# Performance work log

Hardware: AMD Instinct MI355X
Metric: run time of the kernel (lower is better)

The kernel has to match this reference:

```python
import jax, jax.numpy as jnp
import numpy as np

TEMPERATURE = 0.05
EPS = 1e-8  # torch.nn.CosineSimilarity eps


def setup_inputs() -> dict:
    key = jax.random.key(0)
    k1, k2 = jax.random.split(key)
    z1 = jax.random.normal(k1, (8192, 512), dtype=jnp.float32)
    z2 = jax.random.normal(k2, (8192, 512), dtype=jnp.float32)
    return {"z1": z1, "z2": z2}


def reference(z1, z2):
    # Pairwise cosine similarity via GEMM on raw dots / outer product of norms,
    # matching torch CosineSimilarity: dot / max(||a||*||b||, eps).
    dots = jnp.einsum('id,jd->ij', z1, z2)          # [N, N]
    n1 = jnp.linalg.norm(z1, axis=-1)               # [N]
    n2 = jnp.linalg.norm(z2, axis=-1)               # [N]
    denom = jnp.maximum(n1[:, None] * n2[None, :], EPS)
    sim = dots / denom / TEMPERATURE                # [N, N]
    return -jnp.mean(jax.scipy.special.logsumexp(sim, axis=-1))
```

## Files before the change

kernel.cpp:

```cpp
#include <hip/hip_runtime.h>
#include <hip/hip_bf16.h>

#define NROW 8192
#define DDIM 512
#define TEMP_INV 20.0f
#define SHIFT 20.0f

#define BM 256
#define BN 256
#define BK 64
#define KT (DDIM / BK)
#define TILE_A_ELE (BM * BK)
#define BUF_ELE (2 * TILE_A_ELE)
#define LDS_BYTES (2 * BUF_ELE * 2)

typedef __attribute__((ext_vector_type(8))) short short8;
typedef __attribute__((ext_vector_type(4))) float f32x4;

__device__ __forceinline__ void gload16(const __hip_bfloat16* g, __hip_bfloat16* l) {
  __builtin_amdgcn_global_load_lds(
      (const __attribute__((address_space(1))) void*)g,
      (__attribute__((address_space(3))) void*)l,
      16, 0, 0);
}

__global__ __launch_bounds__(256) void normalize_rows(
    const float* __restrict__ z1, const float* __restrict__ z2,
    __hip_bfloat16* __restrict__ z1n, __hip_bfloat16* __restrict__ z2n,
    float* __restrict__ rowsum) {
  int row = blockIdx.x * 4 + (threadIdx.x >> 6);
  int lane = threadIdx.x & 63;

  const float* src;
  __hip_bfloat16* dst;
  float numer;
  if (row < NROW) {
    src = z1 + (size_t)row * DDIM;
    dst = z1n + (size_t)row * DDIM;
    numer = TEMP_INV;
    if (lane == 0) rowsum[row] = 0.0f;
  } else {
    int r = row - NROW;
    src = z2 + (size_t)r * DDIM;
    dst = z2n + (size_t)r * DDIM;
    numer = 1.0f;
  }

  float4 v0 = *reinterpret_cast<const float4*>(src + lane * 8);
  float4 v1 = *reinterpret_cast<const float4*>(src + lane * 8 + 4);
  float ss = v0.x * v0.x + v0.y * v0.y + v0.z * v0.z + v0.w * v0.w +
             v1.x * v1.x + v1.y * v1.y + v1.z * v1.z + v1.w * v1.w;
#pragma unroll
  for (int off = 32; off; off >>= 1) ss += __shfl_xor(ss, off);

  float scale = numer / fmaxf(sqrtf(ss), 1e-8f);

  float vals[8] = {v0.x, v0.y, v0.z, v0.w, v1.x, v1.y, v1.z, v1.w};
  union { __hip_bfloat16 h[8]; uint4 q; } pk;
#pragma unroll
  for (int j = 0; j < 8; ++j) pk.h[j] = __float2bfloat16(vals[j] * scale);
  *reinterpret_cast<uint4*>(dst + lane * 8) = pk.q;
}

#define VMC(N) asm volatile("s_waitcnt vmcnt(" #N ")" ::: "memory")
#define SBAR()                          \
  do {                                  \
    __builtin_amdgcn_s_barrier();       \
    __builtin_amdgcn_sched_barrier(0);  \
  } while (0)

#define LDSA(BUFB, QM, MI, KK)                                                \
  (*reinterpret_cast<const short8*>(                                          \
      &lds[(size_t)(BUFB) * BUF_ELE +                                         \
           (wr * 128 + (QM) * 64 + (MI) * 16 + l15) * BK +                    \
           ((((KK) * 4 + hi) ^ x7) * 8)]))
#define LDSB(BUFB, QN, NI, KK)                                                \
  (*reinterpret_cast<const short8*>(                                          \
      &lds[(size_t)(BUFB) * BUF_ELE + TILE_A_ELE +                            \
           (wc * 64 + (QN) * 32 + (NI) * 16 + l15) * BK +                     \
           ((((KK) * 4 + hi) ^ x7) * 8)]))

#define MF4(QM, MI, QN, BF)                                                   \
  acc[(QM) * 4 + (MI)][(QN) * 2 + 0] =                                        \
      __builtin_amdgcn_mfma_f32_16x16x32_bf16(                                \
          af[(MI) * 2 + 0], (BF)[0], acc[(QM) * 4 + (MI)][(QN) * 2 + 0],      \
          0, 0, 0);                                                           \
  acc[(QM) * 4 + (MI)][(QN) * 2 + 0] =                                        \
      __builtin_amdgcn_mfma_f32_16x16x32_bf16(                                \
          af[(MI) * 2 + 1], (BF)[1], acc[(QM) * 4 + (MI)][(QN) * 2 + 0],      \
          0, 0, 0);                                                           \
  acc[(QM) * 4 + (MI)][(QN) * 2 + 1] =                                        \
      __builtin_amdgcn_mfma_f32_16x16x32_bf16(                                \
          af[(MI) * 2 + 0], (BF)[2], acc[(QM) * 4 + (MI)][(QN) * 2 + 1],      \
          0, 0, 0);                                                           \
  acc[(QM) * 4 + (MI)][(QN) * 2 + 1] =                                        \
      __builtin_amdgcn_mfma_f32_16x16x32_bf16(                                \
          af[(MI) * 2 + 1], (BF)[3], acc[(QM) * 4 + (MI)][(QN) * 2 + 1],      \
          0, 0, 0);

#define PHASE_A(BUFB, QM, ST, H)                                              \
  do {                                                                        \
    af[0] = LDSA(BUFB, QM, 0, 0); af[1] = LDSA(BUFB, QM, 0, 1);               \
    af[2] = LDSA(BUFB, QM, 1, 0); af[3] = LDSA(BUFB, QM, 1, 1);               \
    STAGE_HALF(ST, H);                                                        \
    af[4] = LDSA(BUFB, QM, 2, 0); af[5] = LDSA(BUFB, QM, 2, 1);               \
    af[6] = LDSA(BUFB, QM, 3, 0); af[7] = LDSA(BUFB, QM, 3, 1);               \
    SBAR();                                                                   \
    __builtin_amdgcn_s_setprio(1);                                            \
    MF4(QM, 0, 0, bf0) MF4(QM, 1, 0, bf0)                                     \
    MF4(QM, 2, 0, bf0) MF4(QM, 3, 0, bf0)                                     \
    __builtin_amdgcn_s_setprio(0);                                            \
    SBAR();                                                                   \
  } while (0)

#define PHASE_B(BUFB, ST, H)                                                  \
  do {                                                                        \
    bf1[0] = LDSB(BUFB, 1, 0, 0); bf1[1] = LDSB(BUFB, 1, 0, 1);               \
    bf1[2] = LDSB(BUFB, 1, 1, 0); bf1[3] = LDSB(BUFB, 1, 1, 1);               \
    STAGE_HALF(ST, H);                                                        \
    SBAR();                                                                   \
    __builtin_amdgcn_s_setprio(1);                                            \
    MF4(0, 0, 1, bf1) MF4(0, 1, 1, bf1)                                       \
    MF4(0, 2, 1, bf1) MF4(0, 3, 1, bf1)                                       \
    __builtin_amdgcn_s_setprio(0);                                            \
    SBAR();                                                                   \
  } while (0)

#define PHASE_W(ST, PBUF)                                                     \
  do {                                                                        \
    STAGE_HALF(ST, 0);                                                        \
    VMC(2);                                                                   \
    SBAR();                                                                   \
    bf0[0] = LDSB(PBUF, 0, 0, 0); bf0[1] = LDSB(PBUF, 0, 0, 1);               \
    bf0[2] = LDSB(PBUF, 0, 1, 0); bf0[3] = LDSB(PBUF, 0, 1, 1);               \
    __builtin_amdgcn_s_setprio(1);                                            \
    MF4(1, 0, 1, bf1) MF4(1, 1, 1, bf1)                                       \
    MF4(1, 2, 1, bf1) MF4(1, 3, 1, bf1)                                       \
    __builtin_amdgcn_s_setprio(0);                                            \
    SBAR();                                                                   \
  } while (0)

__global__ __launch_bounds__(512, 2) void gemm_lse(
    const __hip_bfloat16* __restrict__ An,
    const __hip_bfloat16* __restrict__ Bn,
    float* __restrict__ rowsum) {
  extern __shared__ __align__(16) __hip_bfloat16 lds[];

  const int bid = blockIdx.x;
  const int chunk = bid & 7;
  const int slot = bid >> 3;
  const int by = chunk * 4 + ((slot >> 2) & 3);
  const int bx = (slot >> 4) * 4 + (slot & 3);
  const int brow = by * BM;
  const int bcol = bx * BN;

  const int tid = threadIdx.x;
  const int w = tid >> 6;
  const int lane = tid & 63;
  const int wr = w >> 2;
  const int wc = w & 3;

  f32x4 acc[8][4];
#pragma unroll
  for (int m = 0; m < 8; ++m)
#pragma unroll
    for (int n = 0; n < 4; ++n) acc[m][n] = (f32x4)0.0f;

  const int srow8 = lane >> 3;
  const int sslot = (lane & 7) ^ srow8;

  auto STAGE_HALF = [&](int st, int h) {
    const int stm = st & (KT - 1);
    const __hip_bfloat16* gbase =
        (h < 2) ? An + (size_t)brow * DDIM : Bn + (size_t)bcol * DDIM;
    const int rowt = (h & 1) * 128 + w * 16;
    const __hip_bfloat16* g =
        gbase + (size_t)(rowt + srow8) * DDIM + stm * BK + sslot * 8;
    __hip_bfloat16* dst = lds + (size_t)(stm & 1) * BUF_ELE +
                          ((h >= 2) ? TILE_A_ELE : 0) + rowt * BK;
    gload16(g, dst);
    gload16(g + (size_t)8 * DDIM, dst + 8 * BK);
  };

  const int hi = lane >> 4;
  const int l15 = lane & 15;
  const int x7 = lane & 7;

  STAGE_HALF(0, 0); STAGE_HALF(0, 1); STAGE_HALF(0, 2); STAGE_HALF(0, 3);
  STAGE_HALF(1, 0);
  VMC(2);
  SBAR();

  short8 af[8], bf0[4], bf1[4];
  bf0[0] = LDSB(0, 0, 0, 0); bf0[1] = LDSB(0, 0, 0, 1);
  bf0[2] = LDSB(0, 0, 1, 0); bf0[3] = LDSB(0, 0, 1, 1);

  for (int i = 0; i < KT / 2; ++i) {
    const int t1 = 2 * i + 1, t2 = 2 * i + 2, t3 = 2 * i + 3;
    PHASE_A(0, 0, t1, 1);
    PHASE_B(0, t1, 2);
    PHASE_A(0, 1, t1, 3);
    PHASE_W(t2, 1);
    PHASE_A(1, 0, t2, 1);
    PHASE_B(1, t2, 2);
    PHASE_A(1, 1, t2, 3);
    PHASE_W(t3, 0);
  }

  const float L2E = 1.4426950408889634f;
  const float NEG = -SHIFT * 1.4426950408889634f;
#pragma unroll
  for (int m = 0; m < 8; ++m) {
#pragma unroll
    for (int r = 0; r < 4; ++r) {
      float s = 0.0f;
#pragma unroll
      for (int n = 0; n < 4; ++n)
        s += exp2f(fmaf(acc[m][n][r], L2E, NEG));
      s += __shfl_xor(s, 1);
      s += __shfl_xor(s, 2);
      s += __shfl_xor(s, 4);
      s += __shfl_xor(s, 8);
      if (l15 == 0)
        atomicAdd(&rowsum[brow + wr * 128 + m * 16 + hi * 4 + r], s);
    }
  }
}

__global__ __launch_bounds__(1024) void finalize_lse(
    const float* __restrict__ rowsum, float* __restrict__ out) {
  __shared__ float sm[16];
  float s = 0.0f;
  for (int i = threadIdx.x; i < NROW; i += 1024) s += logf(rowsum[i]);
#pragma unroll
  for (int off = 32; off; off >>= 1) s += __shfl_xor(s, off);
  int w = threadIdx.x >> 6;
  if ((threadIdx.x & 63) == 0) sm[w] = s;
  __syncthreads();
  if (threadIdx.x == 0) {
    float t = 0.0f;
#pragma unroll
    for (int i = 0; i < 16; ++i) t += sm[i];
    out[0] = -(t / (float)NROW + SHIFT);
  }
}

extern "C" void kernel_launch(void* const* d_in, const int* in_sizes, int n_in,
                              void* d_out, int out_size, void* d_ws,
                              size_t ws_size, hipStream_t stream) {
  const float* z1 = (const float*)d_in[0];
  const float* z2 = (const float*)d_in[1];
  float* out = (float*)d_out;

  char* ws = (char*)d_ws;
  __hip_bfloat16* z1n = (__hip_bfloat16*)ws;
  __hip_bfloat16* z2n = (__hip_bfloat16*)(ws + (size_t)NROW * DDIM * 2);
  float* rowsum = (float*)(ws + (size_t)2 * NROW * DDIM * 2);

  static bool attr_set = false;
  if (!attr_set) {
    hipFuncSetAttribute((const void*)gemm_lse,
                        hipFuncAttributeMaxDynamicSharedMemorySize, LDS_BYTES);
    attr_set = true;
  }

  normalize_rows<<<dim3((2 * NROW) / 4), dim3(256), 0, stream>>>(z1, z2, z1n,
                                                                 z2n, rowsum);
  gemm_lse<<<dim3((NROW / BM) * (NROW / BN)), dim3(512), LDS_BYTES, stream>>>(
      z1n, z2n, rowsum);
  finalize_lse<<<dim3(1), dim3(1024), 0, stream>>>(rowsum, out);
}
```

Baseline: 160.2 us.

## Fuse normalize, GEMM-LSE and finalize into one persistent cooperative kernel

Replaces three kernel launches with one cooperative kernel of 256 blocks that normalizes rows, runs the GEMM with logsumexp epilogue, and reduces the result, separated by grid-wide syncs. Each block now loops over four column tiles, prefetching the next tile's B data across tile boundaries, rather than launching 1024 independent tiles. The final reduction is split into per-block partials plus a single-block sum. This removes launch gaps and tail effects, but it adds grid-sync costs and fixes the grid at one block per co-resident slot, which lowers latency hiding compared with oversubscription.

```diff
diff --git a/kernel.cpp b/kernel.cpp
--- a/kernel.cpp
+++ b/kernel.cpp
@@ -1,5 +1,8 @@
 #include <hip/hip_runtime.h>
 #include <hip/hip_bf16.h>
+#include <hip/hip_cooperative_groups.h>
+
+namespace cg = cooperative_groups;
 
 #define NROW 8192
 #define DDIM 512
@@ -22,44 +25,6 @@
       (const __attribute__((address_space(1))) void*)g,
       (__attribute__((address_space(3))) void*)l,
       16, 0, 0);
-}
-
-__global__ __launch_bounds__(256) void normalize_rows(
-    const float* __restrict__ z1, const float* __restrict__ z2,
-    __hip_bfloat16* __restrict__ z1n, __hip_bfloat16* __restrict__ z2n,
-    float* __restrict__ rowsum) {
-  int row = blockIdx.x * 4 + (threadIdx.x >> 6);
-  int lane = threadIdx.x & 63;
-
-  const float* src;
-  __hip_bfloat16* dst;
-  float numer;
-  if (row < NROW) {
-    src = z1 + (size_t)row * DDIM;
-    dst = z1n + (size_t)row * DDIM;
-    numer = TEMP_INV;
-    if (lane == 0) rowsum[row] = 0.0f;
-  } else {
-    int r = row - NROW;
-    src = z2 + (size_t)r * DDIM;
-    dst = z2n + (size_t)r * DDIM;
-    numer = 1.0f;
-  }
-
-  float4 v0 = *reinterpret_cast<const float4*>(src + lane * 8);
-  float4 v1 = *reinterpret_cast<const float4*>(src + lane * 8 + 4);
-  float ss = v0.x * v0.x + v0.y * v0.y + v0.z * v0.z + v0.w * v0.w +
-             v1.x * v1.x + v1.y * v1.y + v1.z * v1.z + v1.w * v1.w;
-#pragma unroll
-  for (int off = 32; off; off >>= 1) ss += __shfl_xor(ss, off);
-
-  float scale = numer / fmaxf(sqrtf(ss), 1e-8f);
-
-  float vals[8] = {v0.x, v0.y, v0.z, v0.w, v1.x, v1.y, v1.z, v1.w};
-  union { __hip_bfloat16 h[8]; uint4 q; } pk;
-#pragma unroll
-  for (int j = 0; j < 8; ++j) pk.h[j] = __float2bfloat16(vals[j] * scale);
-  *reinterpret_cast<uint4*>(dst + lane * 8) = pk.q;
 }
 
 #define VMC(N) asm volatile("s_waitcnt vmcnt(" #N ")" ::: "memory")
@@ -140,108 +105,158 @@
     SBAR();                                                                   \
   } while (0)
 
-__global__ __launch_bounds__(512, 2) void gemm_lse(
-    const __hip_bfloat16* __restrict__ An,
-    const __hip_bfloat16* __restrict__ Bn,
-    float* __restrict__ rowsum) {
+__global__ __launch_bounds__(512, 2) void fused_contrastive(
+    const float* __restrict__ z1, const float* __restrict__ z2,
+    __hip_bfloat16* __restrict__ z1n, __hip_bfloat16* __restrict__ z2n,
+    float* __restrict__ rowsum, float* __restrict__ partial,
+    float* __restrict__ out) {
   extern __shared__ __align__(16) __hip_bfloat16 lds[];
-
-  const int bid = blockIdx.x;
-  const int chunk = bid & 7;
-  const int slot = bid >> 3;
-  const int by = chunk * 4 + ((slot >> 2) & 3);
-  const int bx = (slot >> 4) * 4 + (slot & 3);
-  const int brow = by * BM;
-  const int bcol = bx * BN;
+  cg::grid_group grid = cg::this_grid();
 
   const int tid = threadIdx.x;
-  const int w = tid >> 6;
   const int lane = tid & 63;
-  const int wr = w >> 2;
-  const int wc = w & 3;
-
-  f32x4 acc[8][4];
-#pragma unroll
-  for (int m = 0; m < 8; ++m)
-#pragma unroll
-    for (int n = 0; n < 4; ++n) acc[m][n] = (f32x4)0.0f;
-
-  const int srow8 = lane >> 3;
-  const int sslot = (lane & 7) ^ srow8;
-
-  auto STAGE_HALF = [&](int st, int h) {
-    const int stm = st & (KT - 1);
-    const __hip_bfloat16* gbase =
-        (h < 2) ? An + (size_t)brow * DDIM : Bn + (size_t)bcol * DDIM;
-    const int rowt = (h & 1) * 128 + w * 16;
-    const __hip_bfloat16* g =
-        gbase + (size_t)(rowt + srow8) * DDIM + stm * BK + sslot * 8;
-    __hip_bfloat16* dst = lds + (size_t)(stm & 1) * BUF_ELE +
-                          ((h >= 2) ? TILE_A_ELE : 0) + rowt * BK;
-    gload16(g, dst);
-    gload16(g + (size_t)8 * DDIM, dst + 8 * BK);
-  };
-
-  const int hi = lane >> 4;
-  const int l15 = lane & 15;
-  const int x7 = lane & 7;
-
-  STAGE_HALF(0, 0); STAGE_HALF(0, 1); STAGE_HALF(0, 2); STAGE_HALF(0, 3);
-  STAGE_HALF(1, 0);
-  VMC(2);
-  SBAR();
-
-  short8 af[8], bf0[4], bf1[4];
-  bf0[0] = LDSB(0, 0, 0, 0); bf0[1] = LDSB(0, 0, 0, 1);
-  bf0[2] = LDSB(0, 0, 1, 0); bf0[3] = LDSB(0, 0, 1, 1);
-
-  for (int i = 0; i < KT / 2; ++i) {
-    const int t1 = 2 * i + 1, t2 = 2 * i + 2, t3 = 2 * i + 3;
-    PHASE_A(0, 0, t1, 1);
-    PHASE_B(0, t1, 2);
-    PHASE_A(0, 1, t1, 3);
-    PHASE_W(t2, 1);
-    PHASE_A(1, 0, t2, 1);
-    PHASE_B(1, t2, 2);
-    PHASE_A(1, 1, t2, 3);
-    PHASE_W(t3, 0);
-  }
-
-  const float L2E = 1.4426950408889634f;
-  const float NEG = -SHIFT * 1.4426950408889634f;
-#pragma unroll
-  for (int m = 0; m < 8; ++m) {
-#pragma unroll
-    for (int r = 0; r < 4; ++r) {
-      float s = 0.0f;
-#pragma unroll
-      for (int n = 0; n < 4; ++n)
-        s += exp2f(fmaf(acc[m][n][r], L2E, NEG));
-      s += __shfl_xor(s, 1);
-      s += __shfl_xor(s, 2);
-      s += __shfl_xor(s, 4);
-      s += __shfl_xor(s, 8);
-      if (l15 == 0)
-        atomicAdd(&rowsum[brow + wr * 128 + m * 16 + hi * 4 + r], s);
+
+  {
+    const int wv = (blockIdx.x << 3) + (tid >> 6);
+    for (int j = 0; j < 8; ++j) {
+      const int row = wv * 8 + j;
+      const float* src;
+      __hip_bfloat16* dst;
+      float numer;
+      if (row < NROW) {
+        src = z1 + (size_t)row * DDIM;
+        dst = z1n + (size_t)row * DDIM;
+        numer = TEMP_INV;
+        if (lane == 0) rowsum[row] = 0.0f;
+      } else {
+        const int r = row - NROW;
+        src = z2 + (size_t)r * DDIM;
+        dst = z2n + (size_t)r * DDIM;
+        numer = 1.0f;
+      }
+      float4 v0 = *reinterpret_cast<const float4*>(src + lane * 8);
+      float4 v1 = *reinterpret_cast<const float4*>(src + lane * 8 + 4);
+      float ss = v0.x * v0.x + v0.y * v0.y + v0.z * v0.z + v0.w * v0.w +
+                 v1.x * v1.x + v1.y * v1.y + v1.z * v1.z + v1.w * v1.w;
+#pragma unroll
+      for (int off = 32; off; off >>= 1) ss += __shfl_xor(ss, off);
+      float scale = numer / fmaxf(sqrtf(ss), 1e-8f);
+      float vals[8] = {v0.x, v0.y, v0.z, v0.w, v1.x, v1.y, v1.z, v1.w};
+      union { __hip_bfloat16 h[8]; uint4 q; } pk;
+#pragma unroll
+      for (int k = 0; k < 8; ++k) pk.h[k] = __float2bfloat16(vals[k] * scale);
+      *reinterpret_cast<uint4*>(dst + lane * 8) = pk.q;
     }
   }
-}
-
-__global__ __launch_bounds__(1024) void finalize_lse(
-    const float* __restrict__ rowsum, float* __restrict__ out) {
-  __shared__ float sm[16];
-  float s = 0.0f;
-  for (int i = threadIdx.x; i < NROW; i += 1024) s += logf(rowsum[i]);
-#pragma unroll
-  for (int off = 32; off; off >>= 1) s += __shfl_xor(s, off);
-  int w = threadIdx.x >> 6;
-  if ((threadIdx.x & 63) == 0) sm[w] = s;
-  __syncthreads();
-  if (threadIdx.x == 0) {
-    float t = 0.0f;
-#pragma unroll
-    for (int i = 0; i < 16; ++i) t += sm[i];
-    out[0] = -(t / (float)NROW + SHIFT);
+  grid.sync();
+
+  {
+    const int xcd = blockIdx.x & 7;
+    const int idx = blockIdx.x >> 3;
+    const int by = xcd * 4 + (idx & 3);
+    const int bxq = idx >> 2;
+    const int brow = by * BM;
+
+    const int w = tid >> 6;
+    const int wr = w >> 2;
+    const int wc = w & 3;
+
+    f32x4 acc[8][4];
+#pragma unroll
+    for (int m = 0; m < 8; ++m)
+#pragma unroll
+      for (int n = 0; n < 4; ++n) acc[m][n] = (f32x4)0.0f;
+
+    const int srow8 = lane >> 3;
+    const int sslot = (lane & 7) ^ srow8;
+
+    int bcol = (bxq * 4) * BN;
+    int bcol_next = bcol + BN;
+
+    auto STAGE_HALF = [&](int st, int h) {
+      const int stm = st & (KT - 1);
+      const int bc = (st >= KT) ? bcol_next : bcol;
+      const __hip_bfloat16* gbase =
+          (h < 2) ? z1n + (size_t)brow * DDIM : z2n + (size_t)bc * DDIM;
+      const int rowt = (h & 1) * 128 + w * 16;
+      const __hip_bfloat16* g =
+          gbase + (size_t)(rowt + srow8) * DDIM + stm * BK + sslot * 8;
+      __hip_bfloat16* dst = lds + (size_t)(stm & 1) * BUF_ELE +
+                            ((h >= 2) ? TILE_A_ELE : 0) + rowt * BK;
+      gload16(g, dst);
+      gload16(g + (size_t)8 * DDIM, dst + 8 * BK);
+    };
+
+    const int hi = lane >> 4;
+    const int l15 = lane & 15;
+    const int x7 = lane & 7;
+
+    short8 af[8], bf0[4], bf1[4];
+
+    STAGE_HALF(0, 0); STAGE_HALF(0, 1); STAGE_HALF(0, 2); STAGE_HALF(0, 3);
+    STAGE_HALF(1, 0);
+    VMC(2);
+    SBAR();
+    bf0[0] = LDSB(0, 0, 0, 0); bf0[1] = LDSB(0, 0, 0, 1);
+    bf0[2] = LDSB(0, 0, 1, 0); bf0[3] = LDSB(0, 0, 1, 1);
+
+    const float L2E = 1.4426950408889634f;
+    const float NEG = -SHIFT * 1.4426950408889634f;
+
+    for (int q = 0; q < 4; ++q) {
+      bcol = (bxq * 4 + q) * BN;
+      bcol_next = (bxq * 4 + ((q + 1) & 3)) * BN;
+
+      for (int i = 0; i < KT / 2; ++i) {
+        const int t1 = 2 * i + 1, t2 = 2 * i + 2, t3 = 2 * i + 3;
+        PHASE_A(0, 0, t1, 1);
+        PHASE_B(0, t1, 2);
+        PHASE_A(0, 1, t1, 3);
+        PHASE_W(t2, 1);
+        PHASE_A(1, 0, t2, 1);
+        PHASE_B(1, t2, 2);
+        PHASE_A(1, 1, t2, 3);
+        PHASE_W(t3, 0);
+      }
+#pragma unroll
+      for (int m = 0; m < 8; ++m) {
+#pragma unroll
+        for (int r = 0; r < 4; ++r) {
+          float s = 0.0f;
+#pragma unroll
+          for (int n = 0; n < 4; ++n)
+            s += exp2f(fmaf(acc[m][n][r], L2E, NEG));
+          s += __shfl_xor(s, 1);
+          s += __shfl_xor(s, 2);
+          s += __shfl_xor(s, 4);
+          s += __shfl_xor(s, 8);
+          if (l15 == 0)
+            atomicAdd(&rowsum[brow + wr * 128 + m * 16 + hi * 4 + r], s);
+        }
+      }
+#pragma unroll
+      for (int m = 0; m < 8; ++m)
+#pragma unroll
+        for (int n = 0; n < 4; ++n) acc[m][n] = (f32x4)0.0f;
+    }
+    VMC(0);
+  }
+  grid.sync();
+
+  if (tid < 64) {
+    float v = (tid < 32) ? logf(rowsum[blockIdx.x * 32 + tid]) : 0.0f;
+#pragma unroll
+    for (int off = 32; off; off >>= 1) v += __shfl_xor(v, off);
+    if (tid == 0) partial[blockIdx.x] = v;
+  }
+  grid.sync();
+
+  if (blockIdx.x == 0 && tid < 64) {
+    float v = 0.0f;
+    for (int i = tid; i < 256; i += 64) v += partial[i];
+#pragma unroll
+    for (int off = 32; off; off >>= 1) v += __shfl_xor(v, off);
+    if (tid == 0) out[0] = -(v / (float)NROW + SHIFT);
   }
 }
 
@@ -256,17 +271,17 @@
   __hip_bfloat16* z1n = (__hip_bfloat16*)ws;
   __hip_bfloat16* z2n = (__hip_bfloat16*)(ws + (size_t)NROW * DDIM * 2);
   float* rowsum = (float*)(ws + (size_t)2 * NROW * DDIM * 2);
+  float* partial = (float*)(ws + (size_t)2 * NROW * DDIM * 2 + NROW * 4);
 
   static bool attr_set = false;
   if (!attr_set) {
-    hipFuncSetAttribute((const void*)gemm_lse,
+    hipFuncSetAttribute((const void*)fused_contrastive,
                         hipFuncAttributeMaxDynamicSharedMemorySize, LDS_BYTES);
     attr_set = true;
   }
 
-  normalize_rows<<<dim3((2 * NROW) / 4), dim3(256), 0, stream>>>(z1, z2, z1n,
-                                                                 z2n, rowsum);
-  gemm_lse<<<dim3((NROW / BM) * (NROW / BN)), dim3(512), LDS_BYTES, stream>>>(
-      z1n, z2n, rowsum);
-  finalize_lse<<<dim3(1), dim3(1024), 0, stream>>>(rowsum, out);
+  void* args[] = {(void*)&z1, (void*)&z2, (void*)&z1n, (void*)&z2n,
+                  (void*)&rowsum, (void*)&partial, (void*)&out};
+  hipLaunchCooperativeKernel((const void*)fused_contrastive, dim3(256),
+                             dim3(512), args, LDS_BYTES, stream);
 }
```

New measurement: 279.8 us. 74.7% more time.

## Switch normalized operands and MFMA to FP8 e4m3 with rescaled epilogue

Applied to the files above, without the earlier changes.

Rows are now normalized, scaled by 20 and quantized to FP8 e4m3 instead of bf16. The GEMM uses fp8 MFMA, which halves operand bytes and global-to-LDS traffic and raises matrix throughput. This requires a new LDS swizzle and staging layout with one 16-byte load per stage, and the epilogue folds the 1/20 rescale into the exp2 coefficient. The cost is large precision loss in the cosine logits before the exponential, which puts the result's tolerance at risk.

```diff
diff --git a/kernel.cpp b/kernel.cpp
--- a/kernel.cpp
+++ b/kernel.cpp
@@ -1,49 +1,51 @@
 #include <hip/hip_runtime.h>
-#include <hip/hip_bf16.h>
+#include <hip/hip_fp8.h>
 
 #define NROW 8192
 #define DDIM 512
-#define TEMP_INV 20.0f
+#define SCALE 20.0f
 #define SHIFT 20.0f
 
 #define BM 256
 #define BN 256
 #define BK 64
 #define KT (DDIM / BK)
-#define TILE_A_ELE (BM * BK)
-#define BUF_ELE (2 * TILE_A_ELE)
-#define LDS_BYTES (2 * BUF_ELE * 2)
-
-typedef __attribute__((ext_vector_type(8))) short short8;
+#define TILE_BYTES (BM * BK)
+#define BUF_BYTES (2 * TILE_BYTES)
+#define LDS_BYTES (2 * BUF_BYTES)
+
 typedef __attribute__((ext_vector_type(4))) float f32x4;
 
-__device__ __forceinline__ void gload16(const __hip_bfloat16* g, __hip_bfloat16* l) {
+__device__ __forceinline__ void gload16(const void* g, void* l) {
   __builtin_amdgcn_global_load_lds(
       (const __attribute__((address_space(1))) void*)g,
       (__attribute__((address_space(3))) void*)l,
       16, 0, 0);
 }
 
+__device__ __forceinline__ unsigned char to_e4m3(float x) {
+  union { __hip_fp8_e4m3 f; unsigned char b; } u;
+  u.f = __hip_fp8_e4m3(x);
+  return u.b;
+}
+
 __global__ __launch_bounds__(256) void normalize_rows(
     const float* __restrict__ z1, const float* __restrict__ z2,
-    __hip_bfloat16* __restrict__ z1n, __hip_bfloat16* __restrict__ z2n,
+    unsigned char* __restrict__ z1n, unsigned char* __restrict__ z2n,
     float* __restrict__ rowsum) {
   int row = blockIdx.x * 4 + (threadIdx.x >> 6);
   int lane = threadIdx.x & 63;
 
   const float* src;
-  __hip_bfloat16* dst;
-  float numer;
+  unsigned char* dst;
   if (row < NROW) {
     src = z1 + (size_t)row * DDIM;
     dst = z1n + (size_t)row * DDIM;
-    numer = TEMP_INV;
     if (lane == 0) rowsum[row] = 0.0f;
   } else {
     int r = row - NROW;
     src = z2 + (size_t)r * DDIM;
     dst = z2n + (size_t)r * DDIM;
-    numer = 1.0f;
   }
 
   float4 v0 = *reinterpret_cast<const float4*>(src + lane * 8);
@@ -53,13 +55,13 @@
 #pragma unroll
   for (int off = 32; off; off >>= 1) ss += __shfl_xor(ss, off);
 
-  float scale = numer / fmaxf(sqrtf(ss), 1e-8f);
+  float scale = SCALE / fmaxf(sqrtf(ss), 1e-8f);
 
   float vals[8] = {v0.x, v0.y, v0.z, v0.w, v1.x, v1.y, v1.z, v1.w};
-  union { __hip_bfloat16 h[8]; uint4 q; } pk;
-#pragma unroll
-  for (int j = 0; j < 8; ++j) pk.h[j] = __float2bfloat16(vals[j] * scale);
-  *reinterpret_cast<uint4*>(dst + lane * 8) = pk.q;
+  union { unsigned char b[8]; unsigned long long q; } pk;
+#pragma unroll
+  for (int j = 0; j < 8; ++j) pk.b[j] = to_e4m3(vals[j] * scale);
+  *reinterpret_cast<unsigned long long*>(dst + lane * 8) = pk.q;
 }
 
 #define VMC(N) asm volatile("s_waitcnt vmcnt(" #N ")" ::: "memory")
@@ -70,31 +72,31 @@
   } while (0)
 
 #define LDSA(BUFB, QM, MI, KK)                                                \
-  (*reinterpret_cast<const short8*>(                                          \
-      &lds[(size_t)(BUFB) * BUF_ELE +                                         \
-           (wr * 128 + (QM) * 64 + (MI) * 16 + l15) * BK +                    \
-           ((((KK) * 4 + hi) ^ x7) * 8)]))
+  (*reinterpret_cast<const long long*>(                                       \
+      &ldsc[(size_t)(BUFB) * BUF_BYTES +                                      \
+            (wr * 128 + (QM) * 64 + (MI) * 16 + l15) * 64 +                   \
+            ((((KK) * 4 + hi) ^ e8) * 8)]))
 #define LDSB(BUFB, QN, NI, KK)                                                \
-  (*reinterpret_cast<const short8*>(                                          \
-      &lds[(size_t)(BUFB) * BUF_ELE + TILE_A_ELE +                            \
-           (wc * 64 + (QN) * 32 + (NI) * 16 + l15) * BK +                     \
-           ((((KK) * 4 + hi) ^ x7) * 8)]))
+  (*reinterpret_cast<const long long*>(                                       \
+      &ldsc[(size_t)(BUFB) * BUF_BYTES + TILE_BYTES +                         \
+            (wc * 64 + (QN) * 32 + (NI) * 16 + l15) * 64 +                    \
+            ((((KK) * 4 + hi) ^ e8) * 8)]))
 
 #define MF4(QM, MI, QN, BF)                                                   \
   acc[(QM) * 4 + (MI)][(QN) * 2 + 0] =                                        \
-      __builtin_amdgcn_mfma_f32_16x16x32_bf16(                                \
+      __builtin_amdgcn_mfma_f32_16x16x32_fp8_fp8(                             \
           af[(MI) * 2 + 0], (BF)[0], acc[(QM) * 4 + (MI)][(QN) * 2 + 0],      \
           0, 0, 0);                                                           \
   acc[(QM) * 4 + (MI)][(QN) * 2 + 0] =                                        \
-      __builtin_amdgcn_mfma_f32_16x16x32_bf16(                                \
+      __builtin_amdgcn_mfma_f32_16x16x32_fp8_fp8(                             \
           af[(MI) * 2 + 1], (BF)[1], acc[(QM) * 4 + (MI)][(QN) * 2 + 0],      \
           0, 0, 0);                                                           \
   acc[(QM) * 4 + (MI)][(QN) * 2 + 1] =                                        \
-      __builtin_amdgcn_mfma_f32_16x16x32_bf16(                                \
+      __builtin_amdgcn_mfma_f32_16x16x32_fp8_fp8(                             \
           af[(MI) * 2 + 0], (BF)[2], acc[(QM) * 4 + (MI)][(QN) * 2 + 1],      \
           0, 0, 0);                                                           \
   acc[(QM) * 4 + (MI)][(QN) * 2 + 1] =                                        \
-      __builtin_amdgcn_mfma_f32_16x16x32_bf16(                                \
+      __builtin_amdgcn_mfma_f32_16x16x32_fp8_fp8(                             \
           af[(MI) * 2 + 1], (BF)[3], acc[(QM) * 4 + (MI)][(QN) * 2 + 1],      \
           0, 0, 0);
 
@@ -129,7 +131,7 @@
 #define PHASE_W(ST, PBUF)                                                     \
   do {                                                                        \
     STAGE_HALF(ST, 0);                                                        \
-    VMC(2);                                                                   \
+    VMC(1);                                                                   \
     SBAR();                                                                   \
     bf0[0] = LDSB(PBUF, 0, 0, 0); bf0[1] = LDSB(PBUF, 0, 0, 1);               \
     bf0[2] = LDSB(PBUF, 0, 1, 0); bf0[3] = LDSB(PBUF, 0, 1, 1);               \
@@ -141,10 +143,10 @@
   } while (0)
 
 __global__ __launch_bounds__(512, 2) void gemm_lse(
-    const __hip_bfloat16* __restrict__ An,
-    const __hip_bfloat16* __restrict__ Bn,
+    const unsigned char* __restrict__ An,
+    const unsigned char* __restrict__ Bn,
     float* __restrict__ rowsum) {
-  extern __shared__ __align__(16) __hip_bfloat16 lds[];
+  extern __shared__ __align__(16) char ldsc[];
 
   const int bid = blockIdx.x;
   const int chunk = bid & 7;
@@ -166,32 +168,31 @@
 #pragma unroll
     for (int n = 0; n < 4; ++n) acc[m][n] = (f32x4)0.0f;
 
-  const int srow8 = lane >> 3;
-  const int sslot = (lane & 7) ^ srow8;
+  const int srow = lane >> 2;
+  const int spair = (lane & 3) ^ ((lane >> 3) & 3);
 
   auto STAGE_HALF = [&](int st, int h) {
     const int stm = st & (KT - 1);
-    const __hip_bfloat16* gbase =
+    const unsigned char* gbase =
         (h < 2) ? An + (size_t)brow * DDIM : Bn + (size_t)bcol * DDIM;
     const int rowt = (h & 1) * 128 + w * 16;
-    const __hip_bfloat16* g =
-        gbase + (size_t)(rowt + srow8) * DDIM + stm * BK + sslot * 8;
-    __hip_bfloat16* dst = lds + (size_t)(stm & 1) * BUF_ELE +
-                          ((h >= 2) ? TILE_A_ELE : 0) + rowt * BK;
+    const unsigned char* g =
+        gbase + (size_t)(rowt + srow) * DDIM + stm * BK + spair * 16;
+    char* dst = ldsc + (size_t)(stm & 1) * BUF_BYTES +
+                ((h >= 2) ? TILE_BYTES : 0) + rowt * 64;
     gload16(g, dst);
-    gload16(g + (size_t)8 * DDIM, dst + 8 * BK);
   };
 
   const int hi = lane >> 4;
   const int l15 = lane & 15;
-  const int x7 = lane & 7;
+  const int e8 = ((l15 >> 1) & 3) << 1;
 
   STAGE_HALF(0, 0); STAGE_HALF(0, 1); STAGE_HALF(0, 2); STAGE_HALF(0, 3);
   STAGE_HALF(1, 0);
-  VMC(2);
+  VMC(1);
   SBAR();
 
-  short8 af[8], bf0[4], bf1[4];
+  long long af[8], bf0[4], bf1[4];
   bf0[0] = LDSB(0, 0, 0, 0); bf0[1] = LDSB(0, 0, 0, 1);
   bf0[2] = LDSB(0, 0, 1, 0); bf0[3] = LDSB(0, 0, 1, 1);
 
@@ -207,7 +208,7 @@
     PHASE_W(t3, 0);
   }
 
-  const float L2E = 1.4426950408889634f;
+  const float L2E20 = 1.4426950408889634f / 20.0f;
   const float NEG = -SHIFT * 1.4426950408889634f;
 #pragma unroll
   for (int m = 0; m < 8; ++m) {
@@ -216,7 +217,7 @@
       float s = 0.0f;
 #pragma unroll
       for (int n = 0; n < 4; ++n)
-        s += exp2f(fmaf(acc[m][n][r], L2E, NEG));
+        s += exp2f(fmaf(acc[m][n][r], L2E20, NEG));
       s += __shfl_xor(s, 1);
       s += __shfl_xor(s, 2);
       s += __shfl_xor(s, 4);
@@ -253,9 +254,9 @@
   float* out = (float*)d_out;
 
   char* ws = (char*)d_ws;
-  __hip_bfloat16* z1n = (__hip_bfloat16*)ws;
-  __hip_bfloat16* z2n = (__hip_bfloat16*)(ws + (size_t)NROW * DDIM * 2);
-  float* rowsum = (float*)(ws + (size_t)2 * NROW * DDIM * 2);
+  unsigned char* z1n = (unsigned char*)ws;
+  unsigned char* z2n = (unsigned char*)(ws + (size_t)NROW * DDIM);
+  float* rowsum = (float*)(ws + (size_t)2 * NROW * DDIM);
 
   static bool attr_set = false;
   if (!attr_set) {
```

Measured after the change: 157.5 us. About the same (-1.7%).
